# Kernel optimization log

Hardware: AMD Instinct MI355X
Metric: run time of the kernel (lower is better)

The kernel has to match this reference:

```python
import jax, jax.numpy as jnp
import numpy as np

LOSS_ALPHA = 0.7  # Config.loss_alpha


def setup_inputs() -> dict:
    key = jax.random.key(0)
    k1, k2, k3 = jax.random.split(key, 3)
    N, D, K = 1024, 256, 65536
    online_emb = jax.random.normal(k1, (N, D), dtype=jnp.float32)
    mom_emb = jax.random.normal(k2, (N, D), dtype=jnp.float32)
    queue = jax.random.normal(k3, (D, K), dtype=jnp.float32)
    temp = jnp.full((1,), 0.07, dtype=jnp.float32)
    return {"online_emb": online_emb, "mom_emb": mom_emb, "queue": queue, "temp": temp}


def _ce_label0(logits):
    # cross-entropy with target class 0 for every row, mean over batch
    return jnp.mean(jax.nn.logsumexp(logits, axis=1) - logits[:, 0])


def reference(online_emb, mom_emb, queue, temp):
    pos_sim = jnp.einsum('nd,nd->n', online_emb, mom_emb)          # [N]
    neg_sim = jnp.einsum('nd,dk->nk', online_emb, queue)           # [N, K]
    logits_raw = jnp.concatenate([pos_sim[:, None], neg_sim], axis=1)  # [N, K+1]
    t = temp[0]
    loss_online = _ce_label0(logits_raw / t)
    loss_momentum = _ce_label0(logits_raw / jax.lax.stop_gradient(t))
    return LOSS_ALPHA * loss_online + (1.0 - LOSS_ALPHA) * loss_momentum
```

## Files before the change

kernel.cpp:

```cpp
#include <hip/hip_runtime.h>
#include <hip/hip_bf16.h>


#define NROWS 1024
#define DDIM  256
#define KQ    65536
#define BN    128
#define NPART 512
#define LN2_F 0.69314718055994531f

typedef short  short8  __attribute__((ext_vector_type(8)));
typedef float  floatx4 __attribute__((ext_vector_type(4)));

__device__ __forceinline__ unsigned short f2bf(float f) {
    unsigned int u = __float_as_uint(f);
    u += 0x7FFFu + ((u >> 16) & 1u);
    return (unsigned short)(u >> 16);
}

#define DPPMOV(x, ctrl) \
    __uint_as_float(__builtin_amdgcn_mov_dpp(__float_as_uint(x), (ctrl), 0xF, 0xF, true))

__device__ __forceinline__ float dpp16_max(float x) {
    x = fmaxf(x, DPPMOV(x, 0xB1));
    x = fmaxf(x, DPPMOV(x, 0x4E));
    x = fmaxf(x, DPPMOV(x, 0x141));
    x = fmaxf(x, DPPMOV(x, 0x140));
    return x;
}
__device__ __forceinline__ float dpp16_sum(float x) {
    x += DPPMOV(x, 0xB1);
    x += DPPMOV(x, 0x4E);
    x += DPPMOV(x, 0x141);
    x += DPPMOV(x, 0x140);
    return x;
}

__global__ __launch_bounds__(256)
void conv_a(const float* __restrict__ A, const float* __restrict__ temp,
            unsigned short* __restrict__ Ab, float* __restrict__ out)
{
    if (blockIdx.x == 0 && threadIdx.x == 0) out[0] = 0.0f;
    const float s = 1.0f / (temp[0] * LN2_F);
    const int i = blockIdx.x * 256 + threadIdx.x;
    const floatx4 v = ((const floatx4*)A)[i];
    ushort4 w;
    w.x = f2bf(v.x * s); w.y = f2bf(v.y * s);
    w.z = f2bf(v.z * s); w.w = f2bf(v.w * s);
    ((ushort4*)Ab)[i] = w;
}

__global__ __launch_bounds__(256, 2)
void gemm_softmax(const unsigned short* __restrict__ Ab,
                  const float* __restrict__ Q,
                  float2* __restrict__ partials)
{
    __shared__ __align__(16) unsigned short Bl[BN * DDIM];

    const int tid  = threadIdx.x;
    const int lane = tid & 63;
    const int wave = tid >> 6;
    const int l15  = lane & 15;
    const int quad = lane >> 4;
    const int nb   = blockIdx.x;
    const int nbase = nb * BN;

    #pragma unroll
    for (int iter = 0; iter < 4; ++iter) {
        const int t2 = iter * 256 + tid;
        const int ny = t2 & 31;
        const int ko = t2 >> 5;
        floatx4 v[8];
        #pragma unroll
        for (int j = 0; j < 8; ++j)
            v[j] = __builtin_nontemporal_load(
                       (const floatx4*)(Q + (size_t)(ko * 8 + j) * KQ + nbase + ny * 4));
        #pragma unroll
        for (int i2 = 0; i2 < 4; ++i2) {
            const int n = ny * 4 + i2;
            const int phys = ko ^ (n & 15);
            short8 w;
            #pragma unroll
            for (int j = 0; j < 8; ++j)
                w[j] = (short)f2bf(v[j][i2]);
            *(short8*)&Bl[n * DDIM + phys * 8] = w;
        }
    }
    __syncthreads();

    #pragma unroll 1
    for (int g = 0; g < 4; ++g) {
        const int rowbase = g * 256 + wave * 64;
        const unsigned short* apb = Ab + (size_t)(rowbase + l15) * DDIM + quad * 8;

        floatx4 acc[4][8] = {};
        short8 afA[4], afB[4], bfA[8], bfB[8];

        #pragma unroll
        for (int i = 0; i < 4; ++i)
            afA[i] = *(const short8*)(apb + i * 16 * DDIM);
        {
            const int vb = l15 * 512 + ((quad ^ l15) * 16);
            #pragma unroll
            for (int j = 0; j < 8; ++j)
                bfA[j] = *(const short8*)((const char*)Bl + vb + j * 8192);
        }

        #pragma unroll 1
        for (int sp = 0; sp < 4; ++sp) {
            const int s1 = 2 * sp + 1;
            #pragma unroll
            for (int i = 0; i < 4; ++i)
                afB[i] = *(const short8*)(apb + i * 16 * DDIM + s1 * 32);
            {
                const int vb = l15 * 512 + (((4 * s1 + quad) ^ l15) * 16);
                #pragma unroll
                for (int j = 0; j < 8; ++j)
                    bfB[j] = *(const short8*)((const char*)Bl + vb + j * 8192);
            }
            #pragma unroll
            for (int i = 0; i < 4; ++i)
                #pragma unroll
                for (int j = 0; j < 8; ++j)
                    acc[i][j] = __builtin_amdgcn_mfma_f32_16x16x32_bf16(afA[i], bfA[j], acc[i][j], 0, 0, 0);

            const int s2 = (2 * sp + 2) & 7;
            #pragma unroll
            for (int i = 0; i < 4; ++i)
                afA[i] = *(const short8*)(apb + i * 16 * DDIM + s2 * 32);
            {
                const int vb = l15 * 512 + (((4 * s2 + quad) ^ l15) * 16);
                #pragma unroll
                for (int j = 0; j < 8; ++j)
                    bfA[j] = *(const short8*)((const char*)Bl + vb + j * 8192);
            }
            #pragma unroll
            for (int i = 0; i < 4; ++i)
                #pragma unroll
                for (int j = 0; j < 8; ++j)
                    acc[i][j] = __builtin_amdgcn_mfma_f32_16x16x32_bf16(afB[i], bfB[j], acc[i][j], 0, 0, 0);
        }

        #pragma unroll
        for (int i = 0; i < 4; ++i) {
            float2 tmp[4];
            #pragma unroll
            for (int r = 0; r < 4; ++r) {
                float mx = acc[i][0][r];
                #pragma unroll
                for (int j = 1; j < 8; ++j) mx = fmaxf(mx, acc[i][j][r]);
                mx = dpp16_max(mx);
                float s2 = 0.f;
                #pragma unroll
                for (int j = 0; j < 8; ++j)
                    s2 += __builtin_amdgcn_exp2f(acc[i][j][r] - mx);
                s2 = dpp16_sum(s2);
                tmp[r] = make_float2(mx, s2);
            }
            if (l15 == 0) {
                const int row = rowbase + i * 16 + quad * 4;
                floatx4* dst = (floatx4*)(partials + (size_t)nb * NROWS + row);
                floatx4 w0 = {tmp[0].x, tmp[0].y, tmp[1].x, tmp[1].y};
                floatx4 w1 = {tmp[2].x, tmp[2].y, tmp[3].x, tmp[3].y};
                __builtin_nontemporal_store(w0, dst);
                __builtin_nontemporal_store(w1, dst + 1);
            }
        }
    }
}

__global__ __launch_bounds__(256)
void finalize_rows(const float2* __restrict__ partials,
                   const float* __restrict__ online,
                   const float* __restrict__ mom,
                   const float* __restrict__ temp,
                   float* __restrict__ out)
{
    const int t = threadIdx.x;
    __shared__ float2 sm[16][17];
    __shared__ float sm_pos[16];

    {
        const float s = 1.0f / (temp[0] * LN2_F);
        const int r2 = t >> 4, c2 = t & 15;
        const float* po = online + (size_t)(blockIdx.x * 16 + r2) * DDIM + c2 * 16;
        const float* pm = mom    + (size_t)(blockIdx.x * 16 + r2) * DDIM + c2 * 16;
        float d = 0.f;
        #pragma unroll
        for (int w = 0; w < 4; ++w) {
            const floatx4 a = *(const floatx4*)(po + w * 4);
            const floatx4 b = *(const floatx4*)(pm + w * 4);
            d += a.x * b.x + a.y * b.y + a.z * b.z + a.w * b.w;
        }
        d = dpp16_sum(d);
        if (c2 == 0) sm_pos[r2] = d * s;
    }

    const int rl  = t & 15;
    const int grp = t >> 4;
    const int row = blockIdx.x * 16 + rl;

    float M = -3.0e38f, S = 0.f;
    #pragma unroll 1
    for (int pb = 0; pb < 32; pb += 8) {
        float2 v[8];
        #pragma unroll
        for (int j = 0; j < 8; ++j)
            v[j] = partials[(size_t)(grp * 32 + pb + j) * NROWS + row];
        #pragma unroll
        for (int j = 0; j < 8; ++j) {
            const float M2 = fmaxf(M, v[j].x);
            S = S * __builtin_amdgcn_exp2f(M - M2) + v[j].y * __builtin_amdgcn_exp2f(v[j].x - M2);
            M = M2;
        }
    }
    sm[grp][rl] = make_float2(M, S);
    __syncthreads();

    if (t < 64) {
        float val = 0.f;
        if (t < 16) {
            float Mm = -3.0e38f, Ss = 0.f;
            #pragma unroll
            for (int g2 = 0; g2 < 16; ++g2) {
                const float2 v = sm[g2][t];
                const float M2 = fmaxf(Mm, v.x);
                Ss = Ss * __builtin_amdgcn_exp2f(Mm - M2) + v.y * __builtin_amdgcn_exp2f(v.x - M2);
                Mm = M2;
            }
            const float p  = sm_pos[t];
            const float M2 = fmaxf(Mm, p);
            const float L  = Ss * __builtin_amdgcn_exp2f(Mm - M2) + __builtin_amdgcn_exp2f(p - M2);
            val = (M2 + __builtin_amdgcn_logf(L) - p) * LN2_F;
        }
        val += __shfl_xor(val, 1, 64);
        val += __shfl_xor(val, 2, 64);
        val += __shfl_xor(val, 4, 64);
        val += __shfl_xor(val, 8, 64);
        val += __shfl_xor(val, 16, 64);
        val += __shfl_xor(val, 32, 64);
        if (t == 0) atomicAdd(out, val * (1.0f / (float)NROWS));
    }
}

extern "C" void kernel_launch(void* const* d_in, const int* in_sizes, int n_in,
                              void* d_out, int out_size, void* d_ws, size_t ws_size,
                              hipStream_t stream)
{
    const float* online = (const float*)d_in[0];
    const float* mom    = (const float*)d_in[1];
    const float* queue  = (const float*)d_in[2];
    const float* temp   = (const float*)d_in[3];
    float* out = (float*)d_out;

    char* ws = (char*)d_ws;
    unsigned short* Ab = (unsigned short*)ws;
    float2* partials   = (float2*)(ws + 524288);

    conv_a<<<256, 256, 0, stream>>>(online, temp, Ab, out);
    gemm_softmax<<<KQ / BN, 256, 0, stream>>>(Ab, queue, partials);
    finalize_rows<<<64, 256, 0, stream>>>(partials, online, mom, temp, out);
}
```

Before: 150.8 us.

## Split queue tile into two halves and overlap second-half staging with compute

Each block still covers 128 queue columns but now loads them as two 64-column halves into double-buffered LDS. Global loads for the second half are issued while the first half's MFMA groups run. Per-row max/sum partials for the first half are kept in LDS and merged with the second half's results before one write to global. This aims to hide the initial queue-load latency that used to sit in front of all compute, at the cost of more LDS (about 72KB per block, which may reduce occupancy), more register pressure, and smaller per-wave MFMA tiles.

```diff
diff --git a/kernel.cpp b/kernel.cpp
--- a/kernel.cpp
+++ b/kernel.cpp
@@ -5,7 +5,7 @@
 #define NROWS 1024
 #define DDIM  256
 #define KQ    65536
-#define BN    128
+#define BN    64
 #define NPART 512
 #define LN2_F 0.69314718055994531f
 
@@ -55,7 +55,8 @@
                   const float* __restrict__ Q,
                   float2* __restrict__ partials)
 {
-    __shared__ __align__(16) unsigned short Bl[BN * DDIM];
+    __shared__ __align__(16) unsigned short Bl[2][BN * DDIM];
+    __shared__ __align__(16) float2 smP[NROWS];
 
     const int tid  = threadIdx.x;
     const int lane = tid & 63;
@@ -63,38 +64,37 @@
     const int l15  = lane & 15;
     const int quad = lane >> 4;
     const int nb   = blockIdx.x;
-    const int nbase = nb * BN;
-
-    #pragma unroll
-    for (int iter = 0; iter < 4; ++iter) {
-        const int t2 = iter * 256 + tid;
-        const int ny = t2 & 31;
-        const int ko = t2 >> 5;
-        floatx4 v[8];
+    const int cb0  = nb * (2 * BN);
+
+    auto stage_issue = [&](int h, int cb, floatx4* v) {
+        const int t2 = h * 256 + tid;
+        const int ny = t2 & 15;
+        const int ko = t2 >> 4;
         #pragma unroll
         for (int j = 0; j < 8; ++j)
             v[j] = __builtin_nontemporal_load(
-                       (const floatx4*)(Q + (size_t)(ko * 8 + j) * KQ + nbase + ny * 4));
+                       (const floatx4*)(Q + (size_t)(ko * 8 + j) * KQ + cb + ny * 4));
+    };
+    auto stage_write = [&](int h, unsigned short* bl, const floatx4* v) {
+        const int t2 = h * 256 + tid;
+        const int ny = t2 & 15;
+        const int ko = t2 >> 4;
         #pragma unroll
         for (int i2 = 0; i2 < 4; ++i2) {
             const int n = ny * 4 + i2;
             const int phys = ko ^ (n & 15);
             short8 w;
             #pragma unroll
-            for (int j = 0; j < 8; ++j)
-                w[j] = (short)f2bf(v[j][i2]);
-            *(short8*)&Bl[n * DDIM + phys * 8] = w;
-        }
-    }
-    __syncthreads();
-
-    #pragma unroll 1
-    for (int g = 0; g < 4; ++g) {
-        const int rowbase = g * 256 + wave * 64;
+            for (int j = 0; j < 8; ++j) w[j] = (short)f2bf(v[j][i2]);
+            *(short8*)&bl[n * DDIM + phys * 8] = w;
+        }
+    };
+
+    auto compute_group = [&](const unsigned short* bl, int rowbase, bool merge) {
         const unsigned short* apb = Ab + (size_t)(rowbase + l15) * DDIM + quad * 8;
-
-        floatx4 acc[4][8] = {};
-        short8 afA[4], afB[4], bfA[8], bfB[8];
+        const char* blc = (const char*)bl;
+        floatx4 acc[4][4] = {};
+        short8 afA[4], afB[4], bfA[4], bfB[4];
 
         #pragma unroll
         for (int i = 0; i < 4; ++i)
@@ -102,10 +102,9 @@
         {
             const int vb = l15 * 512 + ((quad ^ l15) * 16);
             #pragma unroll
-            for (int j = 0; j < 8; ++j)
-                bfA[j] = *(const short8*)((const char*)Bl + vb + j * 8192);
-        }
-
+            for (int j = 0; j < 4; ++j)
+                bfA[j] = *(const short8*)(blc + vb + j * 8192);
+        }
         #pragma unroll 1
         for (int sp = 0; sp < 4; ++sp) {
             const int s1 = 2 * sp + 1;
@@ -115,13 +114,13 @@
             {
                 const int vb = l15 * 512 + (((4 * s1 + quad) ^ l15) * 16);
                 #pragma unroll
-                for (int j = 0; j < 8; ++j)
-                    bfB[j] = *(const short8*)((const char*)Bl + vb + j * 8192);
+                for (int j = 0; j < 4; ++j)
+                    bfB[j] = *(const short8*)(blc + vb + j * 8192);
             }
             #pragma unroll
             for (int i = 0; i < 4; ++i)
                 #pragma unroll
-                for (int j = 0; j < 8; ++j)
+                for (int j = 0; j < 4; ++j)
                     acc[i][j] = __builtin_amdgcn_mfma_f32_16x16x32_bf16(afA[i], bfA[j], acc[i][j], 0, 0, 0);
 
             const int s2 = (2 * sp + 2) & 7;
@@ -131,13 +130,13 @@
             {
                 const int vb = l15 * 512 + (((4 * s2 + quad) ^ l15) * 16);
                 #pragma unroll
-                for (int j = 0; j < 8; ++j)
-                    bfA[j] = *(const short8*)((const char*)Bl + vb + j * 8192);
+                for (int j = 0; j < 4; ++j)
+                    bfA[j] = *(const short8*)(blc + vb + j * 8192);
             }
             #pragma unroll
             for (int i = 0; i < 4; ++i)
                 #pragma unroll
-                for (int j = 0; j < 8; ++j)
+                for (int j = 0; j < 4; ++j)
                     acc[i][j] = __builtin_amdgcn_mfma_f32_16x16x32_bf16(afB[i], bfB[j], acc[i][j], 0, 0, 0);
         }
 
@@ -148,25 +147,69 @@
             for (int r = 0; r < 4; ++r) {
                 float mx = acc[i][0][r];
                 #pragma unroll
-                for (int j = 1; j < 8; ++j) mx = fmaxf(mx, acc[i][j][r]);
+                for (int j = 1; j < 4; ++j) mx = fmaxf(mx, acc[i][j][r]);
                 mx = dpp16_max(mx);
-                float s2 = 0.f;
-                #pragma unroll
-                for (int j = 0; j < 8; ++j)
-                    s2 += __builtin_amdgcn_exp2f(acc[i][j][r] - mx);
-                s2 = dpp16_sum(s2);
-                tmp[r] = make_float2(mx, s2);
+                float s2s = 0.f;
+                #pragma unroll
+                for (int j = 0; j < 4; ++j)
+                    s2s += __builtin_amdgcn_exp2f(acc[i][j][r] - mx);
+                s2s = dpp16_sum(s2s);
+                tmp[r] = make_float2(mx, s2s);
             }
             if (l15 == 0) {
                 const int row = rowbase + i * 16 + quad * 4;
-                floatx4* dst = (floatx4*)(partials + (size_t)nb * NROWS + row);
-                floatx4 w0 = {tmp[0].x, tmp[0].y, tmp[1].x, tmp[1].y};
-                floatx4 w1 = {tmp[2].x, tmp[2].y, tmp[3].x, tmp[3].y};
-                __builtin_nontemporal_store(w0, dst);
-                __builtin_nontemporal_store(w1, dst + 1);
-            }
-        }
+                if (!merge) {
+                    floatx4* dst = (floatx4*)&smP[row];
+                    floatx4 w0 = {tmp[0].x, tmp[0].y, tmp[1].x, tmp[1].y};
+                    floatx4 w1 = {tmp[2].x, tmp[2].y, tmp[3].x, tmp[3].y};
+                    dst[0] = w0; dst[1] = w1;
+                } else {
+                    const floatx4 p0 = ((const floatx4*)&smP[row])[0];
+                    const floatx4 p1 = ((const floatx4*)&smP[row])[1];
+                    const float m0[4] = {p0.x, p0.z, p1.x, p1.z};
+                    const float s0[4] = {p0.y, p0.w, p1.y, p1.w};
+                    float2 o[4];
+                    #pragma unroll
+                    for (int r = 0; r < 4; ++r) {
+                        const float M2 = fmaxf(m0[r], tmp[r].x);
+                        const float S  = s0[r] * __builtin_amdgcn_exp2f(m0[r] - M2)
+                                       + tmp[r].y * __builtin_amdgcn_exp2f(tmp[r].x - M2);
+                        o[r] = make_float2(M2, S);
+                    }
+                    floatx4* dst = (floatx4*)(partials + (size_t)nb * NROWS + row);
+                    floatx4 w0 = {o[0].x, o[0].y, o[1].x, o[1].y};
+                    floatx4 w1 = {o[2].x, o[2].y, o[3].x, o[3].y};
+                    __builtin_nontemporal_store(w0, dst);
+                    __builtin_nontemporal_store(w1, dst + 1);
+                }
+            }
+        }
+    };
+
+    {
+        floatx4 v0[8], v1[8];
+        stage_issue(0, cb0, v0);
+        stage_issue(1, cb0, v1);
+        stage_write(0, &Bl[0][0], v0);
+        stage_write(1, &Bl[0][0], v1);
     }
+    __syncthreads();
+
+    floatx4 sv[8];
+    stage_issue(0, cb0 + BN, sv);
+    compute_group(&Bl[0][0], 0 * 256 + wave * 64, false);
+    stage_write(0, &Bl[1][0], sv);
+    stage_issue(1, cb0 + BN, sv);
+    compute_group(&Bl[0][0], 1 * 256 + wave * 64, false);
+    stage_write(1, &Bl[1][0], sv);
+    compute_group(&Bl[0][0], 2 * 256 + wave * 64, false);
+    compute_group(&Bl[0][0], 3 * 256 + wave * 64, false);
+    __syncthreads();
+
+    compute_group(&Bl[1][0], 0 * 256 + wave * 64, true);
+    compute_group(&Bl[1][0], 1 * 256 + wave * 64, true);
+    compute_group(&Bl[1][0], 2 * 256 + wave * 64, true);
+    compute_group(&Bl[1][0], 3 * 256 + wave * 64, true);
 }
 
 __global__ __launch_bounds__(256)
@@ -258,6 +301,6 @@
     float2* partials   = (float2*)(ws + 524288);
 
     conv_a<<<256, 256, 0, stream>>>(online, temp, Ab, out);
-    gemm_softmax<<<KQ / BN, 256, 0, stream>>>(Ab, queue, partials);
+    gemm_softmax<<<KQ / (2 * BN), 256, 0, stream>>>(Ab, queue, partials);
     finalize_rows<<<64, 256, 0, stream>>>(partials, online, mom, temp, out);
 }
```

After: 176.5 us. +17.1%, slower.

## Use 512-thread blocks with smaller per-wave tiles and drop register double-buffering

Applied to the files above, without the earlier changes.

The GEMM-softmax kernel moves from 4 to 8 waves per block, with each wave now covering 32 rows instead of 64. This halves the accumulator and fragment register footprint, and the manual A/B fragment double-buffering is replaced by a simple single-buffered k loop. The goal is higher occupancy (launch bounds 512,4) and more waves sharing each staged LDS tile of the queue, to hide latency. The cost is losing the explicit load/MFMA software pipelining and re-reading the B fragments from LDS for fewer MFMAs per load.

```diff
diff --git a/kernel.cpp b/kernel.cpp
--- a/kernel.cpp
+++ b/kernel.cpp
@@ -50,7 +50,7 @@
     ((ushort4*)Ab)[i] = w;
 }
 
-__global__ __launch_bounds__(256, 2)
+__global__ __launch_bounds__(512, 4)
 void gemm_softmax(const unsigned short* __restrict__ Ab,
                   const float* __restrict__ Q,
                   float2* __restrict__ partials)
@@ -65,9 +65,9 @@
     const int nb   = blockIdx.x;
     const int nbase = nb * BN;
 
-    #pragma unroll
-    for (int iter = 0; iter < 4; ++iter) {
-        const int t2 = iter * 256 + tid;
+    #pragma unroll 1
+    for (int iter = 0; iter < 2; ++iter) {
+        const int t2 = iter * 512 + tid;
         const int ny = t2 & 31;
         const int ko = t2 >> 5;
         floatx4 v[8];
@@ -90,59 +90,32 @@
 
     #pragma unroll 1
     for (int g = 0; g < 4; ++g) {
-        const int rowbase = g * 256 + wave * 64;
+        const int rowbase = g * 256 + wave * 32;
         const unsigned short* apb = Ab + (size_t)(rowbase + l15) * DDIM + quad * 8;
 
-        floatx4 acc[4][8] = {};
-        short8 afA[4], afB[4], bfA[8], bfB[8];
-
-        #pragma unroll
-        for (int i = 0; i < 4; ++i)
-            afA[i] = *(const short8*)(apb + i * 16 * DDIM);
-        {
-            const int vb = l15 * 512 + ((quad ^ l15) * 16);
-            #pragma unroll
-            for (int j = 0; j < 8; ++j)
-                bfA[j] = *(const short8*)((const char*)Bl + vb + j * 8192);
-        }
+        floatx4 acc[2][8] = {};
+        short8 af[2], bf[8];
 
         #pragma unroll 1
-        for (int sp = 0; sp < 4; ++sp) {
-            const int s1 = 2 * sp + 1;
-            #pragma unroll
-            for (int i = 0; i < 4; ++i)
-                afB[i] = *(const short8*)(apb + i * 16 * DDIM + s1 * 32);
+        for (int s = 0; s < 8; ++s) {
+            #pragma unroll
+            for (int i = 0; i < 2; ++i)
+                af[i] = *(const short8*)(apb + i * 16 * DDIM + s * 32);
             {
-                const int vb = l15 * 512 + (((4 * s1 + quad) ^ l15) * 16);
+                const int vb = l15 * 512 + (((4 * s + quad) ^ l15) * 16);
                 #pragma unroll
                 for (int j = 0; j < 8; ++j)
-                    bfB[j] = *(const short8*)((const char*)Bl + vb + j * 8192);
-            }
-            #pragma unroll
-            for (int i = 0; i < 4; ++i)
+                    bf[j] = *(const short8*)((const char*)Bl + vb + j * 8192);
+            }
+            #pragma unroll
+            for (int i = 0; i < 2; ++i)
                 #pragma unroll
                 for (int j = 0; j < 8; ++j)
-                    acc[i][j] = __builtin_amdgcn_mfma_f32_16x16x32_bf16(afA[i], bfA[j], acc[i][j], 0, 0, 0);
-
-            const int s2 = (2 * sp + 2) & 7;
-            #pragma unroll
-            for (int i = 0; i < 4; ++i)
-                afA[i] = *(const short8*)(apb + i * 16 * DDIM + s2 * 32);
-            {
-                const int vb = l15 * 512 + (((4 * s2 + quad) ^ l15) * 16);
-                #pragma unroll
-                for (int j = 0; j < 8; ++j)
-                    bfA[j] = *(const short8*)((const char*)Bl + vb + j * 8192);
-            }
-            #pragma unroll
-            for (int i = 0; i < 4; ++i)
-                #pragma unroll
-                for (int j = 0; j < 8; ++j)
-                    acc[i][j] = __builtin_amdgcn_mfma_f32_16x16x32_bf16(afB[i], bfB[j], acc[i][j], 0, 0, 0);
-        }
-
-        #pragma unroll
-        for (int i = 0; i < 4; ++i) {
+                    acc[i][j] = __builtin_amdgcn_mfma_f32_16x16x32_bf16(af[i], bf[j], acc[i][j], 0, 0, 0);
+        }
+
+        #pragma unroll
+        for (int i = 0; i < 2; ++i) {
             float2 tmp[4];
             #pragma unroll
             for (int r = 0; r < 4; ++r) {
@@ -258,6 +231,6 @@
     float2* partials   = (float2*)(ws + 524288);
 
     conv_a<<<256, 256, 0, stream>>>(online, temp, Ab, out);
-    gemm_softmax<<<KQ / BN, 256, 0, stream>>>(Ab, queue, partials);
+    gemm_softmax<<<KQ / BN, 512, 0, stream>>>(Ab, queue, partials);
     finalize_rows<<<64, 256, 0, stream>>>(partials, online, mom, temp, out);
 }
```

New measurement: 146.0 us. 3.1% less time.
